# Optimization experiments

Hardware: AMD Instinct MI355X
Metric: run time of the kernel (lower is better)

## Reference

```python
import jax, jax.numpy as jnp
import numpy as np

N, E, G = 10000, 320000, 256
IN_NODE, OUT_NODE, IN_EDGE, HID = 32, 32, 16, 64
BN_EPS = 1e-5


def setup_inputs() -> dict:
    key = jax.random.key(0)
    ks = jax.random.split(key, 8)
    return {
        "x": jax.random.normal(ks[0], (N, IN_NODE), jnp.float32),
        "edge_attr": jax.random.normal(ks[1], (E, IN_EDGE), jnp.float32),
        "edge_index": jax.random.randint(ks[2], (2, E), 0, N),
        "batch": jnp.sort(jax.random.randint(ks[3], (N,), 0, G)),
        "W1": jax.random.normal(ks[4], (IN_EDGE, HID), jnp.float32) * 0.1,
        "b1": jnp.zeros((HID,), jnp.float32),
        "gamma": jnp.ones((HID,), jnp.float32),
        "beta": jnp.zeros((HID,), jnp.float32),
        "W2": jax.random.normal(ks[5], (HID, IN_NODE * OUT_NODE), jnp.float32) * 0.05,
        "b2": jnp.zeros((IN_NODE * OUT_NODE,), jnp.float32),
        "W_root": jax.random.normal(ks[6], (IN_NODE, OUT_NODE), jnp.float32) * 0.1,
        "bias": jnp.zeros((OUT_NODE,), jnp.float32),
        "num_graphs": G,
    }


def reference(x, edge_attr, edge_index, batch, W1, b1, gamma, beta, W2, b2, W_root, bias, num_graphs):
    src, dst = edge_index[0], edge_index[1]
    # edge MLP: Linear -> BatchNorm1d (training-mode batch stats) -> ReLU -> Linear
    h = edge_attr @ W1 + b1                                   # [E, HID]
    mu = jnp.mean(h, axis=0)
    var = jnp.var(h, axis=0)
    h = (h - mu) * jax.lax.rsqrt(var + BN_EPS) * gamma + beta
    h = jax.nn.relu(h)
    w_e = (h @ W2 + b2).reshape(-1, x.shape[1], W_root.shape[1])  # [E, in, out]
    # gather source features, per-edge matmul, scatter-add to targets
    msgs = jnp.einsum('ei,eio->eo', x[src], w_e)              # [E, out]
    aggr = jax.ops.segment_sum(msgs, dst, num_segments=x.shape[0])
    out = aggr + x @ W_root + bias                            # [N, out]
    # global mean pool per graph
    pooled = jax.ops.segment_sum(out, batch, num_segments=num_graphs)
    counts = jax.ops.segment_sum(jnp.ones((x.shape[0],), x.dtype), batch, num_segments=num_graphs)
    return pooled / jnp.maximum(counts, 1.0)[:, None]
```

## Files before the change

kernel.cpp:

```cpp
#include <hip/hip_runtime.h>
#include <stdint.h>

typedef unsigned short u16;
typedef _Float16 f16x2 __attribute__((ext_vector_type(2)));
typedef _Float16 v8h  __attribute__((ext_vector_type(8)));
typedef float    v4f  __attribute__((ext_vector_type(4)));
union U32F16 { uint32_t u; f16x2 h; };
union ABFrag { uint32_t u[4]; v8h h; };

__device__ __forceinline__ float bf2f(u16 v) {
    union { uint32_t u; float f; } c; c.u = ((uint32_t)v) << 16; return c.f;
}
__device__ __forceinline__ u16 f2bf(float f) {
    union { uint32_t u; float f; } c; c.f = f;
    uint32_t u = c.u;
    return (u16)((u + 0x7FFF + ((u >> 16) & 1)) >> 16);
}
__device__ __forceinline__ float loadf(const void* p, size_t i, int isbf) {
    return isbf ? bf2f(((const u16*)p)[i]) : ((const float*)p)[i];
}
__device__ __forceinline__ int get_isbf(const void* gamma) {
    return ((const uint32_t*)gamma)[0] != 0x3F800000u;
}
#define LGKM_WAIT() __asm__ volatile("s_waitcnt lgkmcnt(0)" ::: "memory")

__global__ __launch_bounds__(256) void k_moments(
    const void* __restrict__ ea, const int* __restrict__ eidx,
    float* __restrict__ mom, int* __restrict__ cntn,
    const void* __restrict__ gamma, int E) {
    int isbf = get_isbf(gamma);
    __shared__ float ea_s[128][17];
    int t = threadIdx.x;
    int ii = 0, jj = 0;
    if (t >= 16 && t < 152) {
        int p = t - 16, i2 = 0;
        while (p >= 16 - i2) { p -= 16 - i2; i2++; }
        ii = i2; jj = i2 + p;
    }
    float acc = 0.f;
    int ntiles = (E + 127) >> 7;
    for (int tile = blockIdx.x; tile < ntiles; tile += gridDim.x) {
        int e0 = tile * 128;
        int cnt = min(128, E - e0);
        if (!isbf) {
            for (int u = t; u < 512; u += 256) {
                int el = u >> 2, q = u & 3;
                if (el < cnt) {
                    float4 v = *(const float4*)((const float*)ea + (size_t)(e0 + el) * 16 + q * 4);
                    ea_s[el][q * 4 + 0] = v.x; ea_s[el][q * 4 + 1] = v.y;
                    ea_s[el][q * 4 + 2] = v.z; ea_s[el][q * 4 + 3] = v.w;
                }
            }
        } else {
            int el = t >> 1, q = t & 1;
            if (el < cnt) {
                uint4 v = *(const uint4*)((const u16*)ea + (size_t)(e0 + el) * 16 + q * 8);
                const u16* h8 = (const u16*)&v;
#pragma unroll
                for (int m = 0; m < 8; m++) ea_s[el][q * 8 + m] = bf2f(h8[m]);
            }
        }
        if (t < cnt) atomicAdd(&cntn[eidx[e0 + t]], 1);
        __syncthreads();
        if (t < 16) {
            for (int e = 0; e < cnt; e++) acc += ea_s[e][t];
        } else if (t < 152) {
            for (int e = 0; e < cnt; e++) acc += ea_s[e][ii] * ea_s[e][jj];
        }
        __syncthreads();
    }
    if (t < 152) atomicAdd(&mom[t], acc);
}

__global__ __launch_bounds__(256) void k_scanprep(
    const float* __restrict__ mom,
    const void* __restrict__ W1, const void* __restrict__ b1,
    const void* __restrict__ gamma, const void* __restrict__ beta,
    const int* __restrict__ cntn, int* __restrict__ offsets,
    float* __restrict__ W1eff, float* __restrict__ b1eff, int N, float invE) {
    __shared__ float M[16][16], S[16];
    __shared__ int ssum[256];
    int t = threadIdx.x;
    int isbf = get_isbf(gamma);
    if (t < 16) S[t] = mom[t];
    if (t >= 16 && t < 152) {
        int p = t - 16, i2 = 0;
        while (p >= 16 - i2) { p -= 16 - i2; i2++; }
        float v = mom[t];
        M[i2][i2 + p] = v; M[i2 + p][i2] = v;
    }
    __syncthreads();
    if (t < 64) {
        int k = t;
        float w[16];
#pragma unroll
        for (int i = 0; i < 16; i++) w[i] = loadf(W1, (size_t)i * 64 + k, isbf);
        float s1 = 0.f;
#pragma unroll
        for (int i = 0; i < 16; i++) s1 += w[i] * S[i];
        s1 *= invE;
        float s2 = 0.f;
#pragma unroll
        for (int i = 0; i < 16; i++) {
            float r = 0.f;
#pragma unroll
            for (int j = 0; j < 16; j++) r += w[j] * M[i][j];
            s2 += w[i] * r;
        }
        s2 *= invE;
        float bk = loadf(b1, k, isbf);
        float mu = s1 + bk;
        float var = s2 - s1 * s1;
        float a = loadf(gamma, k, isbf) * rsqrtf(var + 1e-5f);
        b1eff[k] = bk * a + loadf(beta, k, isbf) - mu * a;
#pragma unroll
        for (int i = 0; i < 16; i++) W1eff[i * 64 + k] = w[i] * a;
    }
    int chunk = (N + 255) >> 8;
    int lo = min(t * chunk, N), hi = min(lo + chunk, N);
    int s = 0;
    for (int i = lo; i < hi; i++) s += cntn[i];
    ssum[t] = s; __syncthreads();
    for (int d = 1; d < 256; d <<= 1) {
        int v = (t >= d) ? ssum[t - d] : 0;
        __syncthreads();
        ssum[t] += v;
        __syncthreads();
    }
    int run = ssum[t] - s;
    for (int i = lo; i < hi; i++) { offsets[i] = run; run += cntn[i]; }
    if (t == 255) offsets[N] = run;
}

__global__ __launch_bounds__(256) void k_place(
    const int* __restrict__ eidx, const int* __restrict__ offsets,
    int* __restrict__ cursor, int2* __restrict__ eg,
    const int* __restrict__ batch, int E) {
    int e = blockIdx.x * 256 + threadIdx.x;
    if (e < E) {
        int s = eidx[e];
        int pos = offsets[s] + atomicAdd(&cursor[s], 1);
        int g = batch[eidx[E + e]];
        eg[pos] = make_int2(e, g);
    }
}

__global__ __launch_bounds__(256, 3) void k_nodeQ(
    const void* __restrict__ ea, const int2* __restrict__ eg,
    const void* __restrict__ x, const void* __restrict__ W2, const void* __restrict__ b2,
    const float* __restrict__ W1eff, const float* __restrict__ b1eff,
    const int* __restrict__ offsets, float* __restrict__ pooledA8,
    const void* __restrict__ gamma, int N, int E, int G) {
    __shared__ int offs[5];
    __shared__ float xs[4][32], Rs[4][32];
    __shared__ uint32_t Qp[4][32 * 33];
    __shared__ alignas(16) float eaw[4][16 * 20];
    __shared__ uint32_t hwb[4][16 * 33];
    int t = threadIdx.x;
    int n0 = blockIdx.x * 4;
    if (t < 5) offs[t] = offsets[min(n0 + t, N)];
    int isbf = get_isbf(gamma);
    if (t < 128) {
        int nn = t >> 5, i = t & 31;
        int n = n0 + nn;
        xs[nn][i] = (n < N) ? loadf(x, (size_t)n * 32 + i, isbf) : 0.f;
    }
    __syncthreads();
    if (offs[0] == offs[4]) return;

    {
        int o = t & 31, j2 = t >> 5;
        if (!isbf) {
            const float* W2f = (const float*)W2;
            for (int m = 0; m < 4; m++) {
                int jp = j2 + 8 * m;
                size_t base = (size_t)(2 * jp) * 1024 + o;
                float a[4][2];
#pragma unroll
                for (int nn = 0; nn < 4; nn++) { a[nn][0] = 0.f; a[nn][1] = 0.f; }
#pragma unroll 4
                for (int i = 0; i < 32; i++) {
                    float w0 = W2f[base + i * 32];
                    float w1 = W2f[base + 1024 + i * 32];
#pragma unroll
                    for (int nn = 0; nn < 4; nn++) {
                        float xv = xs[nn][i];
                        a[nn][0] += xv * w0; a[nn][1] += xv * w1;
                    }
                }
#pragma unroll
                for (int nn = 0; nn < 4; nn++) {
                    U32F16 p; p.h.x = (_Float16)a[nn][0]; p.h.y = (_Float16)a[nn][1];
                    Qp[nn][jp * 33 + o] = p.u;
                }
            }
        } else {
            const u16* W2h = (const u16*)W2;
            for (int m = 0; m < 4; m++) {
                int jp = j2 + 8 * m;
                size_t base = (size_t)(2 * jp) * 1024 + o;
                float a[4][2];
#pragma unroll
                for (int nn = 0; nn < 4; nn++) { a[nn][0] = 0.f; a[nn][1] = 0.f; }
#pragma unroll 4
                for (int i = 0; i < 32; i++) {
                    float w0 = bf2f(W2h[base + i * 32]);
                    float w1 = bf2f(W2h[base + 1024 + i * 32]);
#pragma unroll
                    for (int nn = 0; nn < 4; nn++) {
                        float xv = xs[nn][i];
                        a[nn][0] += xv * w0; a[nn][1] += xv * w1;
                    }
                }
#pragma unroll
                for (int nn = 0; nn < 4; nn++) {
                    U32F16 p; p.h.x = (_Float16)a[nn][0]; p.h.y = (_Float16)a[nn][1];
                    Qp[nn][jp * 33 + o] = p.u;
                }
            }
        }
    }
    if (t < 128) {
        int nn = t >> 5, o = t & 31;
        float acc = 0.f;
#pragma unroll 8
        for (int i = 0; i < 32; i++) acc += xs[nn][i] * loadf(b2, (size_t)i * 32 + o, isbf);
        Rs[nn][o] = acc;
    }
    __syncthreads();

    int w = t >> 6, lane = t & 63;
    int lo = offs[w], hi = offs[w + 1];
    int q = lane >> 4, c = lane & 15;
    int half = lane >> 5, kp = lane & 31;
    uint32_t bfr[2][2][4];
#pragma unroll
    for (int kh = 0; kh < 2; kh++)
#pragma unroll
        for (int oh = 0; oh < 2; oh++)
#pragma unroll
            for (int jj = 0; jj < 4; jj++)
                bfr[kh][oh][jj] = Qp[w][(kh * 16 + q * 4 + jj) * 33 + oh * 16 + c];
    float Rv2[2] = { Rs[w][c], Rs[w][16 + c] };
    float w1a[16], w1b[16];
#pragma unroll
    for (int i = 0; i < 16; i++) {
        w1a[i] = W1eff[i * 64 + 2 * kp];
        w1b[i] = W1eff[i * 64 + 2 * kp + 1];
    }
    float bka = b1eff[2 * kp], bkb = b1eff[2 * kp + 1];
    float* poolbase = pooledA8 + (size_t)(blockIdx.x & 7) * G * 32;

    if (lo >= hi) return;

    int2 egc = make_int2(-1, 0), egn = make_int2(-1, 0);
    { int j = lo + (lane & 15); if (lane < 16 && j < hi) egc = eg[j]; }
    { int j = lo + 16 + (lane & 15); if (lane < 16 && j < hi) egn = eg[j]; }
    float4 eaf = make_float4(0, 0, 0, 0);
    uint4  eab = make_uint4(0, 0, 0, 0);
    if (!isbf) {
        int es = __shfl(egc.x, lane >> 2);
        if (es >= 0) eaf = *(const float4*)((const float*)ea + (size_t)es * 16 + (lane & 3) * 4);
    } else {
        int es = __shfl(egc.x, lane >> 1);
        if (lane < 32 && es >= 0) eab = *(const uint4*)((const u16*)ea + (size_t)es * 16 + (lane & 1) * 8);
    }

    for (int j0 = lo; j0 < hi; j0 += 16) {
        int nvalid = min(16, hi - j0);
        if (!isbf) {
            int m = lane >> 2, qq = lane & 3;
            *(float4*)&eaw[w][m * 20 + qq * 4] = eaf;
        } else if (lane < 32) {
            int m = lane >> 1, hh = lane & 1;
            const u16* h8 = (const u16*)&eab;
            float4 f0 = make_float4(bf2f(h8[0]), bf2f(h8[1]), bf2f(h8[2]), bf2f(h8[3]));
            float4 f1 = make_float4(bf2f(h8[4]), bf2f(h8[5]), bf2f(h8[6]), bf2f(h8[7]));
            *(float4*)&eaw[w][m * 20 + hh * 8] = f0;
            *(float4*)&eaw[w][m * 20 + hh * 8 + 4] = f1;
        }
        int2 eg2 = make_int2(-1, 0);
        { int j = j0 + 32 + (lane & 15); if (lane < 16 && j < hi) eg2 = eg[j]; }
        float4 eaf_n = make_float4(0, 0, 0, 0);
        uint4  eab_n = make_uint4(0, 0, 0, 0);
        if (!isbf) {
            int es = __shfl(egn.x, lane >> 2);
            if (es >= 0) eaf_n = *(const float4*)((const float*)ea + (size_t)es * 16 + (lane & 3) * 4);
        } else {
            int es = __shfl(egn.x, lane >> 1);
            if (lane < 32 && es >= 0) eab_n = *(const uint4*)((const u16*)ea + (size_t)es * 16 + (lane & 1) * 8);
        }
        LGKM_WAIT();
#pragma unroll
        for (int m8 = 0; m8 < 8; m8++) {
            int e = half + 2 * m8;
            if (e < nvalid) {
                float ee[16];
                const float4* ep = (const float4*)&eaw[w][e * 20];
                *(float4*)&ee[0] = ep[0]; *(float4*)&ee[4] = ep[1];
                *(float4*)&ee[8] = ep[2]; *(float4*)&ee[12] = ep[3];
                float va = bka, vb = bkb;
#pragma unroll
                for (int i = 0; i < 16; i++) { va += ee[i] * w1a[i]; vb += ee[i] * w1b[i]; }
                U32F16 ph;
                ph.h.x = (_Float16)fmaxf(va, 0.f);
                ph.h.y = (_Float16)fmaxf(vb, 0.f);
                hwb[w][e * 33 + kp] = ph.u;
            }
        }
        LGKM_WAIT();
        ABFrag a0, a1;
#pragma unroll
        for (int jj = 0; jj < 4; jj++) {
            a0.u[jj] = hwb[w][c * 33 + q * 4 + jj];
            a1.u[jj] = hwb[w][c * 33 + 16 + q * 4 + jj];
        }
#pragma unroll
        for (int oh = 0; oh < 2; oh++) {
            ABFrag b0, b1f;
#pragma unroll
            for (int jj = 0; jj < 4; jj++) { b0.u[jj] = bfr[0][oh][jj]; b1f.u[jj] = bfr[1][oh][jj]; }
            v4f d = {0.f, 0.f, 0.f, 0.f};
            d = __builtin_amdgcn_mfma_f32_16x16x32_f16(a0.h, b0.h, d, 0, 0, 0);
            d = __builtin_amdgcn_mfma_f32_16x16x32_f16(a1.h, b1f.h, d, 0, 0, 0);
#pragma unroll
            for (int r = 0; r < 4; r++) {
                int e = q * 4 + r;
                int g = __shfl(egc.y, e);
                if (e < nvalid)
                    atomicAdd(poolbase + (size_t)g * 32 + oh * 16 + c, d[r] + Rv2[oh]);
            }
        }
        egc = egn; egn = eg2; eaf = eaf_n; eab = eab_n;
    }
}

__global__ __launch_bounds__(256) void k_final(
    const float* __restrict__ pooledA8, const void* __restrict__ x,
    const int* __restrict__ batch, const void* __restrict__ Wr,
    const void* __restrict__ bias, void* __restrict__ out,
    const void* __restrict__ gamma, int N, int G) {
    __shared__ float px[8][32];
    __shared__ float Sx[32];
    int g = blockIdx.x;
    int t = threadIdx.x, row = t >> 5, o = t & 31;
    int isbf = get_isbf(gamma);
    int slo = 0, shi = N;
    { int a = 0, b = N; while (a < b) { int m = (a + b) >> 1; if (batch[m] < g) a = m + 1; else b = m; } slo = a; }
    { int a = slo, b = N; while (a < b) { int m = (a + b) >> 1; if (batch[m] < g + 1) a = m + 1; else b = m; } shi = a; }
    float acc = 0.f;
    for (int n = slo + row; n < shi; n += 8) acc += loadf(x, (size_t)n * 32 + o, isbf);
    px[row][o] = acc;
    __syncthreads();
    if (t < 32) {
        float s = 0.f;
#pragma unroll
        for (int r = 0; r < 8; r++) s += px[r][t];
        Sx[t] = s;
    }
    __syncthreads();
    if (t < 32) {
        float v = 0.f;
#pragma unroll
        for (int sh = 0; sh < 8; sh++) v += pooledA8[((size_t)sh * G + g) * 32 + t];
#pragma unroll 8
        for (int i = 0; i < 32; i++) v += Sx[i] * loadf(Wr, (size_t)i * 32 + t, isbf);
        int cnt = shi - slo;
        v += (float)cnt * loadf(bias, t, isbf);
        v /= (float)max(cnt, 1);
        if (isbf) ((u16*)out)[g * 32 + t] = f2bf(v);
        else ((float*)out)[g * 32 + t] = v;
    }
}

extern "C" void kernel_launch(void* const* d_in, const int* in_sizes, int n_in,
                              void* d_out, int out_size, void* d_ws, size_t ws_size,
                              hipStream_t stream) {
    const void* x    = d_in[0];
    const void* ea   = d_in[1];
    const int* eidx  = (const int*)d_in[2];
    const int* batch = (const int*)d_in[3];
    const void* W1   = d_in[4];
    const void* b1   = d_in[5];
    const void* gamma= d_in[6];
    const void* beta = d_in[7];
    const void* W2   = d_in[8];
    const void* b2   = d_in[9];
    const void* Wr   = d_in[10];
    const void* bias = d_in[11];

    int N = in_sizes[0] / 32;
    int E = in_sizes[1] / 16;
    int G = out_size / 32;

    char* ws = (char*)d_ws;
    size_t off = 0;
    auto alloc = [&](size_t bytes) {
        char* p = ws + off;
        off = (off + bytes + 255) & ~(size_t)255;
        return p;
    };
    float* mom      = (float*)alloc(152 * 4);
    float* pooledA8 = (float*)alloc((size_t)8 * G * 32 * 4);
    int*   cntn     = (int*)alloc((size_t)N * 4);
    int*   cursor   = (int*)alloc((size_t)N * 4);
    size_t zero_bytes = off;
    int*   offsets  = (int*)alloc((size_t)(N + 1) * 4);
    int2*  eg       = (int2*)alloc((size_t)E * 8);
    float* W1eff    = (float*)alloc(1024 * 4);
    float* b1eff    = (float*)alloc(64 * 4);
    (void)ws_size; (void)n_in;

    hipMemsetAsync(d_ws, 0, zero_bytes, stream);
    k_moments<<<256, 256, 0, stream>>>(ea, eidx, mom, cntn, gamma, E);
    k_scanprep<<<1, 256, 0, stream>>>(mom, W1, b1, gamma, beta, cntn, offsets,
                                      W1eff, b1eff, N, 1.0f / (float)E);
    k_place<<<(E + 255) / 256, 256, 0, stream>>>(eidx, offsets, cursor, eg, batch, E);
    k_nodeQ<<<(N + 3) / 4, 256, 0, stream>>>(ea, eg, x, W2, b2, W1eff, b1eff,
                                             offsets, pooledA8, gamma, N, E, G);
    k_final<<<G, 256, 0, stream>>>(pooledA8, x, batch, Wr, bias, d_out, gamma, N, G);
}
```

Baseline: 253.8 us.

## Use MFMA for edge moments and pack weights to fp16 for node kernel

The edge-attribute moment kernel now packs tiles to fp16 in shared memory and computes the Gram matrix and column sums with MFMA instructions instead of a per-thread scalar loop. W2 is pre-packed to fp16 pairs inside the placement kernel, and W1 is packed the same way in the scan kernel, which halves weight loads in the node kernel. The edge MLP first layer now uses fdot2 on fp16 data instead of fp32 FMAs. Occupancy is raised (launch bounds 4) and the moments grid is doubled. Rounding moments and W1 to fp16 adds precision risk to the BatchNorm statistics.

After: 350.0 us. +37.9%, slower.

```diff
diff --git a/kernel.cpp b/kernel.cpp
--- a/kernel.cpp
+++ b/kernel.cpp
@@ -3,10 +3,12 @@
 
 typedef unsigned short u16;
 typedef _Float16 f16x2 __attribute__((ext_vector_type(2)));
-typedef _Float16 v8h  __attribute__((ext_vector_type(8)));
-typedef float    v4f  __attribute__((ext_vector_type(4)));
+typedef _Float16 v4h __attribute__((ext_vector_type(4)));
+typedef _Float16 v8h __attribute__((ext_vector_type(8)));
+typedef float v4f __attribute__((ext_vector_type(4)));
 union U32F16 { uint32_t u; f16x2 h; };
 union ABFrag { uint32_t u[4]; v8h h; };
+union ABFrag4 { uint32_t u[2]; v4h h; };
 
 __device__ __forceinline__ float bf2f(u16 v) {
     union { uint32_t u; float f; } c; c.u = ((uint32_t)v) << 16; return c.f;
@@ -16,11 +18,31 @@
     uint32_t u = c.u;
     return (u16)((u + 0x7FFF + ((u >> 16) & 1)) >> 16);
 }
+__device__ __forceinline__ u16 f2h_bits(float f) {
+    union { _Float16 h; u16 u; } c; c.h = (_Float16)f; return c.u;
+}
+__device__ __forceinline__ uint32_t pack16(float a, float b) {
+    U32F16 p; p.h.x = (_Float16)a; p.h.y = (_Float16)b; return p.u;
+}
 __device__ __forceinline__ float loadf(const void* p, size_t i, int isbf) {
     return isbf ? bf2f(((const u16*)p)[i]) : ((const float*)p)[i];
 }
 __device__ __forceinline__ int get_isbf(const void* gamma) {
     return ((const uint32_t*)gamma)[0] != 0x3F800000u;
+}
+
+#if defined(__has_builtin)
+#if __has_builtin(__builtin_amdgcn_fdot2)
+#define HAS_FDOT2 1
+#endif
+#endif
+__device__ __forceinline__ float fdot2acc(uint32_t a, uint32_t b, float c) {
+    U32F16 ua, ub; ua.u = a; ub.u = b;
+#ifdef HAS_FDOT2
+    return __builtin_amdgcn_fdot2(ua.h, ub.h, c, false);
+#else
+    return c + (float)ua.h.x * (float)ub.h.x + (float)ua.h.y * (float)ub.h.y;
+#endif
 }
 #define LGKM_WAIT() __asm__ volatile("s_waitcnt lgkmcnt(0)" ::: "memory")
 
@@ -29,47 +51,62 @@
     float* __restrict__ mom, int* __restrict__ cntn,
     const void* __restrict__ gamma, int E) {
     int isbf = get_isbf(gamma);
-    __shared__ float ea_s[128][17];
+    __shared__ uint32_t eapk[16 * 65];
     int t = threadIdx.x;
-    int ii = 0, jj = 0;
-    if (t >= 16 && t < 152) {
-        int p = t - 16, i2 = 0;
-        while (p >= 16 - i2) { p -= 16 - i2; i2++; }
-        ii = i2; jj = i2 + p;
-    }
-    float acc = 0.f;
+    int lane = t & 63, w = t >> 6;
+    int q = lane >> 4, c = lane & 15;
+    v4f D = {0.f, 0.f, 0.f, 0.f};
+    v4f S = {0.f, 0.f, 0.f, 0.f};
+    ABFrag4 ones; ones.u[0] = 0x3C003C00u; ones.u[1] = 0x3C003C00u;
+    u16* base = (u16*)eapk;
     int ntiles = (E + 127) >> 7;
     for (int tile = blockIdx.x; tile < ntiles; tile += gridDim.x) {
         int e0 = tile * 128;
         int cnt = min(128, E - e0);
+        __syncthreads();
         if (!isbf) {
             for (int u = t; u < 512; u += 256) {
-                int el = u >> 2, q = u & 3;
-                if (el < cnt) {
-                    float4 v = *(const float4*)((const float*)ea + (size_t)(e0 + el) * 16 + q * 4);
-                    ea_s[el][q * 4 + 0] = v.x; ea_s[el][q * 4 + 1] = v.y;
-                    ea_s[el][q * 4 + 2] = v.z; ea_s[el][q * 4 + 3] = v.w;
-                }
+                int el = u >> 2, qq = u & 3;
+                float4 v = make_float4(0.f, 0.f, 0.f, 0.f);
+                if (el < cnt) v = *(const float4*)((const float*)ea + (size_t)(e0 + el) * 16 + qq * 4);
+                int wrd = el >> 1, hf = el & 1;
+                base[((4 * qq + 0) * 65 + wrd) * 2 + hf] = f2h_bits(v.x);
+                base[((4 * qq + 1) * 65 + wrd) * 2 + hf] = f2h_bits(v.y);
+                base[((4 * qq + 2) * 65 + wrd) * 2 + hf] = f2h_bits(v.z);
+                base[((4 * qq + 3) * 65 + wrd) * 2 + hf] = f2h_bits(v.w);
             }
         } else {
-            int el = t >> 1, q = t & 1;
-            if (el < cnt) {
-                uint4 v = *(const uint4*)((const u16*)ea + (size_t)(e0 + el) * 16 + q * 8);
-                const u16* h8 = (const u16*)&v;
-#pragma unroll
-                for (int m = 0; m < 8; m++) ea_s[el][q * 8 + m] = bf2f(h8[m]);
-            }
+            int el = t >> 1, qq = t & 1;
+            uint4 v = make_uint4(0, 0, 0, 0);
+            if (el < cnt) v = *(const uint4*)((const u16*)ea + (size_t)(e0 + el) * 16 + qq * 8);
+            const u16* h8 = (const u16*)&v;
+            int wrd = el >> 1, hf = el & 1;
+#pragma unroll
+            for (int m = 0; m < 8; m++)
+                base[((8 * qq + m) * 65 + wrd) * 2 + hf] =
+                    (el < cnt) ? f2h_bits(bf2f(h8[m])) : (u16)0;
         }
         if (t < cnt) atomicAdd(&cntn[eidx[e0 + t]], 1);
         __syncthreads();
-        if (t < 16) {
-            for (int e = 0; e < cnt; e++) acc += ea_s[e][t];
-        } else if (t < 152) {
-            for (int e = 0; e < cnt; e++) acc += ea_s[e][ii] * ea_s[e][jj];
-        }
-        __syncthreads();
-    }
-    if (t < 152) atomicAdd(&mom[t], acc);
+#pragma unroll
+        for (int ch = 0; ch < 2; ch++) {
+            int eb2 = w * 16 + ch * 8;
+            ABFrag4 A;
+            A.u[0] = eapk[c * 65 + eb2 + 2 * q];
+            A.u[1] = eapk[c * 65 + eb2 + 2 * q + 1];
+            D = __builtin_amdgcn_mfma_f32_16x16x16f16(A.h, A.h, D, 0, 0, 0);
+            S = __builtin_amdgcn_mfma_f32_16x16x16f16(A.h, ones.h, S, 0, 0, 0);
+        }
+    }
+#pragma unroll
+    for (int r = 0; r < 4; r++) {
+        int i = q * 4 + r, j = c;
+        if (i <= j) {
+            int p = i * 16 - (i * (i - 1)) / 2 + (j - i);
+            atomicAdd(&mom[16 + p], D[r]);
+        }
+        if (c == 0) atomicAdd(&mom[i], S[r]);
+    }
 }
 
 __global__ __launch_bounds__(256) void k_scanprep(
@@ -77,12 +114,12 @@
     const void* __restrict__ W1, const void* __restrict__ b1,
     const void* __restrict__ gamma, const void* __restrict__ beta,
     const int* __restrict__ cntn, int* __restrict__ offsets,
-    float* __restrict__ W1eff, float* __restrict__ b1eff, int N, float invE) {
-    __shared__ float M[16][16], S[16];
+    uint32_t* __restrict__ W1p, float* __restrict__ b1eff, int N, float invE) {
+    __shared__ float M[16][16], Ss[16];
     __shared__ int ssum[256];
     int t = threadIdx.x;
     int isbf = get_isbf(gamma);
-    if (t < 16) S[t] = mom[t];
+    if (t < 16) Ss[t] = mom[t];
     if (t >= 16 && t < 152) {
         int p = t - 16, i2 = 0;
         while (p >= 16 - i2) { p -= 16 - i2; i2++; }
@@ -97,7 +134,7 @@
         for (int i = 0; i < 16; i++) w[i] = loadf(W1, (size_t)i * 64 + k, isbf);
         float s1 = 0.f;
 #pragma unroll
-        for (int i = 0; i < 16; i++) s1 += w[i] * S[i];
+        for (int i = 0; i < 16; i++) s1 += w[i] * Ss[i];
         s1 *= invE;
         float s2 = 0.f;
 #pragma unroll
@@ -114,11 +151,13 @@
         float a = loadf(gamma, k, isbf) * rsqrtf(var + 1e-5f);
         b1eff[k] = bk * a + loadf(beta, k, isbf) - mu * a;
 #pragma unroll
-        for (int i = 0; i < 16; i++) W1eff[i * 64 + k] = w[i] * a;
+        for (int ip = 0; ip < 8; ip++)
+            W1p[k * 8 + ip] = pack16(w[2 * ip] * a, w[2 * ip + 1] * a);
     }
     int chunk = (N + 255) >> 8;
     int lo = min(t * chunk, N), hi = min(lo + chunk, N);
     int s = 0;
+#pragma unroll 4
     for (int i = lo; i < hi; i++) s += cntn[i];
     ssum[t] = s; __syncthreads();
     for (int d = 1; d < 256; d <<= 1) {
@@ -135,26 +174,35 @@
 __global__ __launch_bounds__(256) void k_place(
     const int* __restrict__ eidx, const int* __restrict__ offsets,
     int* __restrict__ cursor, int2* __restrict__ eg,
-    const int* __restrict__ batch, int E) {
-    int e = blockIdx.x * 256 + threadIdx.x;
-    if (e < E) {
-        int s = eidx[e];
+    const int* __restrict__ batch, const void* __restrict__ W2,
+    uint32_t* __restrict__ W2p, const void* __restrict__ gamma, int E) {
+    int idx = blockIdx.x * 256 + threadIdx.x;
+    if (idx < E) {
+        int s = eidx[idx];
         int pos = offsets[s] + atomicAdd(&cursor[s], 1);
-        int g = batch[eidx[E + e]];
-        eg[pos] = make_int2(e, g);
-    }
-}
-
-__global__ __launch_bounds__(256, 3) void k_nodeQ(
+        int g = batch[eidx[E + idx]];
+        eg[pos] = make_int2(idx, g);
+    }
+    if (idx < 32768) {
+        int isbf = get_isbf(gamma);
+        int jp = idx >> 10, io = idx & 1023;
+        float v0 = loadf(W2, (size_t)(2 * jp) * 1024 + io, isbf);
+        float v1 = loadf(W2, (size_t)(2 * jp + 1) * 1024 + io, isbf);
+        W2p[idx] = pack16(v0, v1);
+    }
+}
+
+__global__ __launch_bounds__(256, 4) void k_nodeQ(
     const void* __restrict__ ea, const int2* __restrict__ eg,
-    const void* __restrict__ x, const void* __restrict__ W2, const void* __restrict__ b2,
-    const float* __restrict__ W1eff, const float* __restrict__ b1eff,
-    const int* __restrict__ offsets, float* __restrict__ pooledA8,
-    const void* __restrict__ gamma, int N, int E, int G) {
+    const void* __restrict__ x, const uint32_t* __restrict__ W2p,
+    const void* __restrict__ b2, const uint32_t* __restrict__ W1p,
+    const float* __restrict__ b1eff, const int* __restrict__ offsets,
+    float* __restrict__ pooledA8, const void* __restrict__ gamma,
+    int N, int E, int G) {
     __shared__ int offs[5];
     __shared__ float xs[4][32], Rs[4][32];
     __shared__ uint32_t Qp[4][32 * 33];
-    __shared__ alignas(16) float eaw[4][16 * 20];
+    __shared__ alignas(16) uint32_t eapk2[4][16 * 8];
     __shared__ uint32_t hwb[4][16 * 33];
     int t = threadIdx.x;
     int n0 = blockIdx.x * 4;
@@ -170,55 +218,28 @@
 
     {
         int o = t & 31, j2 = t >> 5;
-        if (!isbf) {
-            const float* W2f = (const float*)W2;
+        float acc[4][4][2];
+#pragma unroll
+        for (int m = 0; m < 4; m++)
+#pragma unroll
+            for (int nn = 0; nn < 4; nn++) { acc[m][nn][0] = 0.f; acc[m][nn][1] = 0.f; }
+        for (int i = 0; i < 32; i++) {
+            float x0 = xs[0][i], x1 = xs[1][i], x2 = xs[2][i], x3 = xs[3][i];
+#pragma unroll
             for (int m = 0; m < 4; m++) {
-                int jp = j2 + 8 * m;
-                size_t base = (size_t)(2 * jp) * 1024 + o;
-                float a[4][2];
-#pragma unroll
-                for (int nn = 0; nn < 4; nn++) { a[nn][0] = 0.f; a[nn][1] = 0.f; }
-#pragma unroll 4
-                for (int i = 0; i < 32; i++) {
-                    float w0 = W2f[base + i * 32];
-                    float w1 = W2f[base + 1024 + i * 32];
-#pragma unroll
-                    for (int nn = 0; nn < 4; nn++) {
-                        float xv = xs[nn][i];
-                        a[nn][0] += xv * w0; a[nn][1] += xv * w1;
-                    }
-                }
-#pragma unroll
-                for (int nn = 0; nn < 4; nn++) {
-                    U32F16 p; p.h.x = (_Float16)a[nn][0]; p.h.y = (_Float16)a[nn][1];
-                    Qp[nn][jp * 33 + o] = p.u;
-                }
+                U32F16 wp; wp.u = W2p[(size_t)(j2 + 8 * m) * 1024 + i * 32 + o];
+                float w0 = (float)wp.h.x, w1 = (float)wp.h.y;
+                acc[m][0][0] += x0 * w0; acc[m][0][1] += x0 * w1;
+                acc[m][1][0] += x1 * w0; acc[m][1][1] += x1 * w1;
+                acc[m][2][0] += x2 * w0; acc[m][2][1] += x2 * w1;
+                acc[m][3][0] += x3 * w0; acc[m][3][1] += x3 * w1;
             }
-        } else {
-            const u16* W2h = (const u16*)W2;
-            for (int m = 0; m < 4; m++) {
-                int jp = j2 + 8 * m;
-                size_t base = (size_t)(2 * jp) * 1024 + o;
-                float a[4][2];
-#pragma unroll
-                for (int nn = 0; nn < 4; nn++) { a[nn][0] = 0.f; a[nn][1] = 0.f; }
-#pragma unroll 4
-                for (int i = 0; i < 32; i++) {
-                    float w0 = bf2f(W2h[base + i * 32]);
-                    float w1 = bf2f(W2h[base + 1024 + i * 32]);
-#pragma unroll
-                    for (int nn = 0; nn < 4; nn++) {
-                        float xv = xs[nn][i];
-                        a[nn][0] += xv * w0; a[nn][1] += xv * w1;
-                    }
-                }
-#pragma unroll
-                for (int nn = 0; nn < 4; nn++) {
-                    U32F16 p; p.h.x = (_Float16)a[nn][0]; p.h.y = (_Float16)a[nn][1];
-                    Qp[nn][jp * 33 + o] = p.u;
-                }
-            }
-        }
+        }
+#pragma unroll
+        for (int m = 0; m < 4; m++)
+#pragma unroll
+            for (int nn = 0; nn < 4; nn++)
+                Qp[nn][(j2 + 8 * m) * 33 + (t & 31)] = pack16(acc[m][nn][0], acc[m][nn][1]);
     }
     if (t < 128) {
         int nn = t >> 5, o = t & 31;
@@ -242,11 +263,11 @@
             for (int jj = 0; jj < 4; jj++)
                 bfr[kh][oh][jj] = Qp[w][(kh * 16 + q * 4 + jj) * 33 + oh * 16 + c];
     float Rv2[2] = { Rs[w][c], Rs[w][16 + c] };
-    float w1a[16], w1b[16];
-#pragma unroll
-    for (int i = 0; i < 16; i++) {
-        w1a[i] = W1eff[i * 64 + 2 * kp];
-        w1b[i] = W1eff[i * 64 + 2 * kp + 1];
+    uint32_t w1pa[8], w1pb[8];
+#pragma unroll
+    for (int ip = 0; ip < 8; ip++) {
+        w1pa[ip] = W1p[(2 * kp) * 8 + ip];
+        w1pb[ip] = W1p[(2 * kp + 1) * 8 + ip];
     }
     float bka = b1eff[2 * kp], bkb = b1eff[2 * kp + 1];
     float* poolbase = pooledA8 + (size_t)(blockIdx.x & 7) * G * 32;
@@ -269,15 +290,20 @@
     for (int j0 = lo; j0 < hi; j0 += 16) {
         int nvalid = min(16, hi - j0);
         if (!isbf) {
-            int m = lane >> 2, qq = lane & 3;
-            *(float4*)&eaw[w][m * 20 + qq * 4] = eaf;
+            int el = lane >> 2, qq = lane & 3;
+            uint2 pk;
+            pk.x = (uint32_t)f2h_bits(eaf.x) | ((uint32_t)f2h_bits(eaf.y) << 16);
+            pk.y = (uint32_t)f2h_bits(eaf.z) | ((uint32_t)f2h_bits(eaf.w) << 16);
+            *(uint2*)&eapk2[w][el * 8 + qq * 2] = pk;
         } else if (lane < 32) {
-            int m = lane >> 1, hh = lane & 1;
+            int el = lane >> 1, hh = lane & 1;
             const u16* h8 = (const u16*)&eab;
-            float4 f0 = make_float4(bf2f(h8[0]), bf2f(h8[1]), bf2f(h8[2]), bf2f(h8[3]));
-            float4 f1 = make_float4(bf2f(h8[4]), bf2f(h8[5]), bf2f(h8[6]), bf2f(h8[7]));
-            *(float4*)&eaw[w][m * 20 + hh * 8] = f0;
-            *(float4*)&eaw[w][m * 20 + hh * 8 + 4] = f1;
+            uint4 pk4;
+            pk4.x = (uint32_t)f2h_bits(bf2f(h8[0])) | ((uint32_t)f2h_bits(bf2f(h8[1])) << 16);
+            pk4.y = (uint32_t)f2h_bits(bf2f(h8[2])) | ((uint32_t)f2h_bits(bf2f(h8[3])) << 16);
+            pk4.z = (uint32_t)f2h_bits(bf2f(h8[4])) | ((uint32_t)f2h_bits(bf2f(h8[5])) << 16);
+            pk4.w = (uint32_t)f2h_bits(bf2f(h8[6])) | ((uint32_t)f2h_bits(bf2f(h8[7])) << 16);
+            *(uint4*)&eapk2[w][el * 8 + hh * 4] = pk4;
         }
         int2 eg2 = make_int2(-1, 0);
         { int j = j0 + 32 + (lane & 15); if (lane < 16 && j < hi) eg2 = eg[j]; }
@@ -295,17 +321,18 @@
         for (int m8 = 0; m8 < 8; m8++) {
             int e = half + 2 * m8;
             if (e < nvalid) {
-                float ee[16];
-                const float4* ep = (const float4*)&eaw[w][e * 20];
-                *(float4*)&ee[0] = ep[0]; *(float4*)&ee[4] = ep[1];
-                *(float4*)&ee[8] = ep[2]; *(float4*)&ee[12] = ep[3];
+                const uint4* ep = (const uint4*)&eapk2[w][e * 8];
+                uint4 p0 = ep[0], p1 = ep[1];
                 float va = bka, vb = bkb;
-#pragma unroll
-                for (int i = 0; i < 16; i++) { va += ee[i] * w1a[i]; vb += ee[i] * w1b[i]; }
-                U32F16 ph;
-                ph.h.x = (_Float16)fmaxf(va, 0.f);
-                ph.h.y = (_Float16)fmaxf(vb, 0.f);
-                hwb[w][e * 33 + kp] = ph.u;
+                va = fdot2acc(p0.x, w1pa[0], va); va = fdot2acc(p0.y, w1pa[1], va);
+                va = fdot2acc(p0.z, w1pa[2], va); va = fdot2acc(p0.w, w1pa[3], va);
+                va = fdot2acc(p1.x, w1pa[4], va); va = fdot2acc(p1.y, w1pa[5], va);
+                va = fdot2acc(p1.z, w1pa[6], va); va = fdot2acc(p1.w, w1pa[7], va);
+                vb = fdot2acc(p0.x, w1pb[0], vb); vb = fdot2acc(p0.y, w1pb[1], vb);
+                vb = fdot2acc(p0.z, w1pb[2], vb); vb = fdot2acc(p0.w, w1pb[3], vb);
+                vb = fdot2acc(p1.x, w1pb[4], vb); vb = fdot2acc(p1.y, w1pb[5], vb);
+                vb = fdot2acc(p1.z, w1pb[6], vb); vb = fdot2acc(p1.w, w1pb[7], vb);
+                hwb[w][e * 33 + kp] = pack16(fmaxf(va, 0.f), fmaxf(vb, 0.f));
             }
         }
         LGKM_WAIT();
@@ -405,18 +432,20 @@
     int*   cntn     = (int*)alloc((size_t)N * 4);
     int*   cursor   = (int*)alloc((size_t)N * 4);
     size_t zero_bytes = off;
-    int*   offsets  = (int*)alloc((size_t)(N + 1) * 4);
-    int2*  eg       = (int2*)alloc((size_t)E * 8);
-    float* W1eff    = (float*)alloc(1024 * 4);
-    float* b1eff    = (float*)alloc(64 * 4);
+    int*      offsets = (int*)alloc((size_t)(N + 1) * 4);
+    int2*     eg      = (int2*)alloc((size_t)E * 8);
+    uint32_t* W1p     = (uint32_t*)alloc(64 * 8 * 4);
+    float*    b1eff   = (float*)alloc(64 * 4);
+    uint32_t* W2p     = (uint32_t*)alloc(32768 * 4);
     (void)ws_size; (void)n_in;
 
     hipMemsetAsync(d_ws, 0, zero_bytes, stream);
-    k_moments<<<256, 256, 0, stream>>>(ea, eidx, mom, cntn, gamma, E);
+    k_moments<<<512, 256, 0, stream>>>(ea, eidx, mom, cntn, gamma, E);
     k_scanprep<<<1, 256, 0, stream>>>(mom, W1, b1, gamma, beta, cntn, offsets,
-                                      W1eff, b1eff, N, 1.0f / (float)E);
-    k_place<<<(E + 255) / 256, 256, 0, stream>>>(eidx, offsets, cursor, eg, batch, E);
-    k_nodeQ<<<(N + 3) / 4, 256, 0, stream>>>(ea, eg, x, W2, b2, W1eff, b1eff,
+                                      W1p, b1eff, N, 1.0f / (float)E);
+    k_place<<<(E + 255) / 256, 256, 0, stream>>>(eidx, offsets, cursor, eg, batch,
+                                                 W2, W2p, gamma, E);
+    k_nodeQ<<<(N + 3) / 4, 256, 0, stream>>>(ea, eg, x, W2p, b2, W1p, b1eff,
                                              offsets, pooledA8, gamma, N, E, G);
     k_final<<<G, 256, 0, stream>>>(pooledA8, x, batch, Wr, bias, d_out, gamma, N, G);
 }
```
